# Performance work log

Hardware: AMD Instinct MI355X
Metric: run time of the kernel (lower is better)

Reference implementation:

```python
import jax, jax.numpy as jnp
import numpy as np

B, N, R = 16, 512, 10
DE, DR, DOUT = 256, 64, 256

def setup_inputs() -> dict:
    key = jax.random.key(0)
    k1, k2, k3, k4 = jax.random.split(key, 4)
    node_features = jax.random.normal(k1, (B, N, DE), dtype=jnp.float32)
    relation_features = jax.random.normal(k2, (B, R, DR), dtype=jnp.float32)
    adj = jax.random.uniform(k3, (B, R, N, N), dtype=jnp.float32)
    in_dim = (DE + DR) * R
    bound = float(np.sqrt(6.0 / (in_dim + DOUT)))  # xavier_uniform
    W = jax.random.uniform(k4, (DOUT, in_dim), dtype=jnp.float32, minval=-bound, maxval=bound)
    bias = jnp.zeros((DOUT,), dtype=jnp.float32)
    return {"node_features": node_features, "relation_features": relation_features,
            "adj": adj, "W": W, "bias": bias}

def reference(node_features, relation_features, adj, W, bias):
    # adj: [B,R,N,N]; node_features: [B,N,De]; relation_features: [B,R,Dr]
    # Per relation r: bmm(adj[:,r], cat([node, rel_r broadcast], -1))
    # Node part: adj @ node_features for every relation at once.
    node_part = jnp.einsum('brnm,bmd->brnd', adj, node_features)      # [B,R,N,De]
    # Relation part: adj @ (rel_r repeated over rows) == rowsum(adj) * rel_r
    rel_part = adj.sum(axis=-1)[..., None] * relation_features[:, :, None, :]  # [B,R,N,Dr]
    supports = jnp.concatenate([node_part, rel_part], axis=-1)        # [B,R,N,De+Dr]
    supports = supports.transpose(0, 2, 1, 3).reshape(node_features.shape[0],
                                                      node_features.shape[1], -1)  # [B,N,R*(De+Dr)]
    return supports @ W.T + bias
```

## Files before the change

kernel.cpp:

```cpp
#include <hip/hip_runtime.h>
#include <stdint.h>

#define B_     16
#define N_     512
#define R_     10
#define DE_    256
#define DR_    64
#define DOUT_  256
#define INDIM_ 3200
#define BLK_   320
#define RN_    5120
#define SPLITS_ 4
#define CPS_    20

typedef __bf16          v8bf  __attribute__((ext_vector_type(8)));
typedef unsigned short  v8us  __attribute__((ext_vector_type(8)));
typedef unsigned short  v4us  __attribute__((ext_vector_type(4)));
typedef float           f32x4 __attribute__((ext_vector_type(4)));

static __device__ __forceinline__ unsigned short f2b(float f) {
  union { float f; unsigned u; } c; c.f = f;
  unsigned r = c.u + 0x7FFFu + ((c.u >> 16) & 1u);
  return (unsigned short)(r >> 16);
}

static __device__ __forceinline__ v8bf us2bf(v8us u) {
  union { v8us u; v8bf b; } c; c.u = u; return c.b;
}

static __device__ __forceinline__ void gl_lds16(const void* g, void* l) {
  __builtin_amdgcn_global_load_lds(
      (const __attribute__((address_space(1))) void*)g,
      (__attribute__((address_space(3))) void*)l, 16, 0, 0);
}

__global__ void prep_all(const float* __restrict__ nf, const float* __restrict__ W,
                         const float* __restrict__ rel,
                         unsigned short* __restrict__ nodeB,
                         unsigned short* __restrict__ WnB,
                         float* __restrict__ Uf) {
  const int bb = blockIdx.x;
  const int tid = threadIdx.x;
  if (bb < 256) {
    const size_t base = (size_t)bb * 8192;
#pragma unroll
    for (int p = 0; p < 4; ++p) {
      size_t off = base + (size_t)p * 2048 + (size_t)tid * 8;
      float4 x = *(const float4*)(nf + off);
      float4 y = *(const float4*)(nf + off + 4);
      v8us u;
      u[0] = f2b(x.x); u[1] = f2b(x.y); u[2] = f2b(x.z); u[3] = f2b(x.w);
      u[4] = f2b(y.x); u[5] = f2b(y.y); u[6] = f2b(y.z); u[7] = f2b(y.w);
      *(v8us*)(nodeB + off) = u;
    }
  } else if (bb < 896) {
    int idx = (bb - 256) * 1024 + tid * 4;
    int r = idx >> 16;
    int o = (idx >> 8) & 255;
    int d = idx & 255;
    float4 x = *(const float4*)(W + (size_t)o * INDIM_ + r * BLK_ + d);
    v4us u;
    u[0] = f2b(x.x); u[1] = f2b(x.y); u[2] = f2b(x.z); u[3] = f2b(x.w);
    *(v4us*)(WnB + idx) = u;
  } else {
    int idx = (bb - 896) * 256 + tid;
    int o  = idx & 255;
    int br = idx >> 8;
    int r  = br % R_;
    const float* rp = rel + (size_t)br * DR_;
    const float* wp = W + (size_t)o * INDIM_ + r * BLK_ + DE_;
    float v = 0.f;
#pragma unroll 8
    for (int d = 0; d < DR_; ++d) v += rp[d] * wp[d];
    Uf[idx] = v;
  }
}

__global__ void stageA_gemm(const unsigned short* __restrict__ nodeB,
                            const unsigned short* __restrict__ WnB,
                            const float* __restrict__ Uf,
                            unsigned short* __restrict__ Gp) {
  __shared__ unsigned short S[128 * 128];
  unsigned short* Al = S;
  unsigned short* Bl = S + 128 * 64;
  const int br = blockIdx.x;
  const int b  = br / R_, r = br % R_;
  const int o0 = blockIdx.y * 128;
  const int m0 = blockIdx.z * 128;
  const int tid  = threadIdx.x;
  const int lane = tid & 63;
  const int wave = tid >> 6;
  const int wm = wave >> 1, wn = wave & 1;
  const int quad = lane >> 4, l16 = lane & 15;

  const unsigned short* Wb = WnB + (size_t)r * (DOUT_ * DE_);
  const unsigned short* Nb = nodeB + (size_t)b * (N_ * DE_);

  f32x4 acc[4][4];
#pragma unroll
  for (int i = 0; i < 4; ++i)
#pragma unroll
    for (int j = 0; j < 4; ++j) acc[i][j] = f32x4{0.f, 0.f, 0.f, 0.f};

  for (int dk = 0; dk < DE_; dk += 64) {
#pragma unroll
    for (int it = 0; it < 4; ++it) {
      int rowblk = it * 32 + wave * 8;
      int rl = rowblk + (lane >> 3);
      int kc = (lane & 7) ^ (rl & 7);
      gl_lds16(Wb + (size_t)(o0 + rl) * DE_ + dk + kc * 8, Al + rowblk * 64);
      gl_lds16(Nb + (size_t)(m0 + rl) * DE_ + dk + kc * 8, Bl + rowblk * 64);
    }
    __syncthreads();
#pragma unroll
    for (int ks = 0; ks < 2; ++ks) {
      const int kb = ks * 4;
      v8bf av[4], bv[4];
#pragma unroll
      for (int mi = 0; mi < 4; ++mi) {
        int m = wm * 64 + mi * 16 + l16;
        av[mi] = us2bf(*(const v8us*)(Al + m * 64 + (((kb + quad) ^ (m & 7)) * 8)));
      }
#pragma unroll
      for (int ni = 0; ni < 4; ++ni) {
        int c = wn * 64 + ni * 16 + l16;
        bv[ni] = us2bf(*(const v8us*)(Bl + c * 64 + (((kb + quad) ^ (c & 7)) * 8)));
      }
#pragma unroll
      for (int mi = 0; mi < 4; ++mi)
#pragma unroll
        for (int ni = 0; ni < 4; ++ni)
          acc[mi][ni] = __builtin_amdgcn_mfma_f32_16x16x32_bf16(av[mi], bv[ni], acc[mi][ni], 0, 0, 0);
    }
    __syncthreads();
  }

#pragma unroll
  for (int mi = 0; mi < 4; ++mi)
#pragma unroll
    for (int t = 0; t < 4; ++t) {
      int o_loc = wm * 64 + mi * 16 + quad * 4 + t;
      float u = Uf[(size_t)br * DOUT_ + o0 + o_loc];
#pragma unroll
      for (int ni = 0; ni < 4; ++ni) {
        int m_loc = wn * 64 + ni * 16 + l16;
        S[o_loc * 128 + m_loc] = f2b(acc[mi][ni][t] + u);
      }
    }
  __syncthreads();
#pragma unroll
  for (int p = 0; p < 8; ++p) {
    int idx16 = p * 2048 + tid * 8;
    int orow = idx16 >> 7;
    int moff = idx16 & 127;
    unsigned short* dst = Gp + ((size_t)(b * DOUT_ + o0 + orow)) * RN_ + r * N_ + m0 + moff;
    *(v8us*)dst = *(const v8us*)(S + idx16);
  }
}

__global__ __launch_bounds__(512, 2)
void stageB_gemm(const float* __restrict__ adj,
                 const unsigned short* __restrict__ Gp,
                 float* __restrict__ part) {
  __shared__ unsigned short SB[2 * 24576];
  const int b  = blockIdx.x;
  const int n0 = blockIdx.y * 128;
  const int sp = blockIdx.z;
  const int tid  = threadIdx.x;
  const int lane = tid & 63;
  const int wave = tid >> 6;
  const int wm = wave >> 2;
  const int wn = wave & 3;
  const int quad = lane >> 4, l16 = lane & 15;

  const float* Ab = adj + (size_t)b * (R_ * N_ * N_);
  const unsigned short* Gb = Gp + (size_t)b * (DOUT_ * RN_);

  f32x4 acc[4][4];
#pragma unroll
  for (int i = 0; i < 4; ++i)
#pragma unroll
    for (int j = 0; j < 4; ++j) acc[i][j] = f32x4{0.f, 0.f, 0.f, 0.f};

  const int ar0 = tid >> 3;
  const int ac8 = tid & 7;
  const int acs = ac8 ^ (ar0 & 7);
  const int brl = wave * 8 + (lane >> 3);
  const int bkc = lane & 7;

  int c = sp * CPS_;

  {
    const int r = c >> 3, m0 = (c & 7) << 6, k0 = c << 6;
    unsigned short* Aln = SB;
    unsigned short* Bln = SB + 128 * 64;
#pragma unroll
    for (int s = 0; s < 4; ++s) {
      int rl = s * 64 + brl;
      int kc = bkc ^ (rl & 7);
      gl_lds16(Gb + (size_t)rl * RN_ + k0 + kc * 8, Bln + (s * 64 + wave * 8) * 64);
    }
    const float* Ap = Ab + ((size_t)r * N_ + n0) * N_ + m0;
    float4 a0 = *(const float4*)(Ap + (size_t)ar0 * N_ + ac8 * 8);
    float4 a1 = *(const float4*)(Ap + (size_t)ar0 * N_ + ac8 * 8 + 4);
    float4 a2 = *(const float4*)(Ap + (size_t)(ar0 + 64) * N_ + ac8 * 8);
    float4 a3 = *(const float4*)(Ap + (size_t)(ar0 + 64) * N_ + ac8 * 8 + 4);
    v8us u0, u1;
    u0[0] = f2b(a0.x); u0[1] = f2b(a0.y); u0[2] = f2b(a0.z); u0[3] = f2b(a0.w);
    u0[4] = f2b(a1.x); u0[5] = f2b(a1.y); u0[6] = f2b(a1.z); u0[7] = f2b(a1.w);
    u1[0] = f2b(a2.x); u1[1] = f2b(a2.y); u1[2] = f2b(a2.z); u1[3] = f2b(a2.w);
    u1[4] = f2b(a3.x); u1[5] = f2b(a3.y); u1[6] = f2b(a3.z); u1[7] = f2b(a3.w);
    *(v8us*)(Aln + ar0 * 64 + acs * 8) = u0;
    *(v8us*)(Aln + (ar0 + 64) * 64 + acs * 8) = u1;
  }
  __syncthreads();

  for (int t = 0; t < CPS_; ++t) {
    unsigned short* Sc = SB + (t & 1) * 24576;
    unsigned short* Sn = SB + ((t & 1) ^ 1) * 24576;
    float4 a0, a1, a2, a3;
    const bool pf = (t + 1 < CPS_);
    if (pf) {
      const int c1 = c + 1;
      const int r = c1 >> 3, m0 = (c1 & 7) << 6, k0 = c1 << 6;
      unsigned short* Bln = Sn + 128 * 64;
#pragma unroll
      for (int s = 0; s < 4; ++s) {
        int rl = s * 64 + brl;
        int kc = bkc ^ (rl & 7);
        gl_lds16(Gb + (size_t)rl * RN_ + k0 + kc * 8, Bln + (s * 64 + wave * 8) * 64);
      }
      const float* Ap = Ab + ((size_t)r * N_ + n0) * N_ + m0;
      a0 = *(const float4*)(Ap + (size_t)ar0 * N_ + ac8 * 8);
      a1 = *(const float4*)(Ap + (size_t)ar0 * N_ + ac8 * 8 + 4);
      a2 = *(const float4*)(Ap + (size_t)(ar0 + 64) * N_ + ac8 * 8);
      a3 = *(const float4*)(Ap + (size_t)(ar0 + 64) * N_ + ac8 * 8 + 4);
    }
    const unsigned short* Alc = Sc;
    const unsigned short* Blc = Sc + 128 * 64;
#pragma unroll
    for (int ks = 0; ks < 2; ++ks) {
      const int kb = ks * 4;
      v8bf av[4], bv[4];
#pragma unroll
      for (int mi = 0; mi < 4; ++mi) {
        int m = wm * 64 + mi * 16 + l16;
        av[mi] = us2bf(*(const v8us*)(Alc + m * 64 + (((kb + quad) ^ (m & 7)) * 8)));
      }
#pragma unroll
      for (int ni = 0; ni < 4; ++ni) {
        int o = wn * 64 + ni * 16 + l16;
        bv[ni] = us2bf(*(const v8us*)(Blc + o * 64 + (((kb + quad) ^ (o & 7)) * 8)));
      }
#pragma unroll
      for (int mi = 0; mi < 4; ++mi)
#pragma unroll
        for (int ni = 0; ni < 4; ++ni)
          acc[mi][ni] = __builtin_amdgcn_mfma_f32_16x16x32_bf16(av[mi], bv[ni], acc[mi][ni], 0, 0, 0);
    }
    if (pf) {
      v8us u0, u1;
      u0[0] = f2b(a0.x); u0[1] = f2b(a0.y); u0[2] = f2b(a0.z); u0[3] = f2b(a0.w);
      u0[4] = f2b(a1.x); u0[5] = f2b(a1.y); u0[6] = f2b(a1.z); u0[7] = f2b(a1.w);
      u1[0] = f2b(a2.x); u1[1] = f2b(a2.y); u1[2] = f2b(a2.z); u1[3] = f2b(a2.w);
      u1[4] = f2b(a3.x); u1[5] = f2b(a3.y); u1[6] = f2b(a3.z); u1[7] = f2b(a3.w);
      *(v8us*)(Sn + ar0 * 64 + acs * 8) = u0;
      *(v8us*)(Sn + (ar0 + 64) * 64 + acs * 8) = u1;
    }
    __syncthreads();
    ++c;
  }

  float* pb = part + (((size_t)sp * B_ + b) * N_) * DOUT_;
#pragma unroll
  for (int mi = 0; mi < 4; ++mi)
#pragma unroll
    for (int t4 = 0; t4 < 4; ++t4) {
      int row = n0 + wm * 64 + mi * 16 + quad * 4 + t4;
#pragma unroll
      for (int ni = 0; ni < 4; ++ni) {
        int col = wn * 64 + ni * 16 + l16;
        pb[(size_t)row * DOUT_ + col] = acc[mi][ni][t4];
      }
    }
}

__global__ void reduce_out(const float* __restrict__ part, const float* __restrict__ bias,
                           float* __restrict__ out) {
  const size_t idx = (size_t)blockIdx.x * 256 + threadIdx.x;
  const size_t stride = (size_t)B_ * N_ * DOUT_ / 4;
  f32x4 a = *(const f32x4*)(bias + (idx & 63) * 4);
#pragma unroll
  for (int s = 0; s < SPLITS_; ++s) {
    f32x4 p = *(const f32x4*)((const float*)part + (stride * s + idx) * 4);
    a += p;
  }
  *(f32x4*)(out + idx * 4) = a;
}

extern "C" void kernel_launch(void* const* d_in, const int* in_sizes, int n_in,
                              void* d_out, int out_size, void* d_ws, size_t ws_size,
                              hipStream_t stream) {
  const float* node = (const float*)d_in[0];
  const float* rel  = (const float*)d_in[1];
  const float* adj  = (const float*)d_in[2];
  const float* W    = (const float*)d_in[3];
  const float* bias = (const float*)d_in[4];
  float* out = (float*)d_out;

  char* ws = (char*)d_ws;
  unsigned short* nodeB = (unsigned short*)(ws);
  unsigned short* WnB   = (unsigned short*)(ws + ((size_t)5 << 20));
  float*          Uf    = (float*)         (ws + ((size_t)7 << 20));
  unsigned short* Gp    = (unsigned short*)(ws + ((size_t)8 << 20));
  float*          part  = (float*)         (ws + ((size_t)48 << 20));

  prep_all<<<dim3(1056), 256, 0, stream>>>(node, W, rel, nodeB, WnB, Uf);
  stageA_gemm<<<dim3(B_ * R_, DOUT_ / 128, N_ / 128), 256, 0, stream>>>(nodeB, WnB, Uf, Gp);
  stageB_gemm<<<dim3(B_, N_ / 128, SPLITS_), 512, 0, stream>>>(adj, Gp, part);
  reduce_out<<<dim3((B_ * N_ * DOUT_ / 4) / 256), 256, 0, stream>>>(part, bias, out);
}
```

Baseline: 291.1 us.

## Double-buffer stage A K-loop and shrink stage B tiles to 64 rows

Stage A now double-buffers its LDS tiles across the four 64-wide K steps, prefetching the next chunk while MFMAs run on the current one. Stage B shrinks the row tile from 128 to 64 with 256-thread blocks, doubling the grid to 512 blocks so more CUs have work. Each wave in stage B now covers 64 output columns. The cost is that each block loads the full 256-column Gp tile for only 64 adjacency rows, so Gp is re-read twice as often.

```diff
diff --git a/kernel.cpp b/kernel.cpp
--- a/kernel.cpp
+++ b/kernel.cpp
@@ -80,9 +80,7 @@
                             const unsigned short* __restrict__ WnB,
                             const float* __restrict__ Uf,
                             unsigned short* __restrict__ Gp) {
-  __shared__ unsigned short S[128 * 128];
-  unsigned short* Al = S;
-  unsigned short* Bl = S + 128 * 64;
+  __shared__ unsigned short S[2 * 16384];
   const int br = blockIdx.x;
   const int b  = br / R_, r = br % R_;
   const int o0 = blockIdx.y * 128;
@@ -102,16 +100,41 @@
 #pragma unroll
     for (int j = 0; j < 4; ++j) acc[i][j] = f32x4{0.f, 0.f, 0.f, 0.f};
 
-  for (int dk = 0; dk < DE_; dk += 64) {
+  const int srl = lane >> 3;
+  const int skc = lane & 7;
+
+  {
+    unsigned short* Al = S;
+    unsigned short* Bl = S + 8192;
 #pragma unroll
     for (int it = 0; it < 4; ++it) {
       int rowblk = it * 32 + wave * 8;
-      int rl = rowblk + (lane >> 3);
-      int kc = (lane & 7) ^ (rl & 7);
-      gl_lds16(Wb + (size_t)(o0 + rl) * DE_ + dk + kc * 8, Al + rowblk * 64);
-      gl_lds16(Nb + (size_t)(m0 + rl) * DE_ + dk + kc * 8, Bl + rowblk * 64);
-    }
-    __syncthreads();
+      int rl = rowblk + srl;
+      int kc = skc ^ (rl & 7);
+      gl_lds16(Wb + (size_t)(o0 + rl) * DE_ + kc * 8, Al + rowblk * 64);
+      gl_lds16(Nb + (size_t)(m0 + rl) * DE_ + kc * 8, Bl + rowblk * 64);
+    }
+  }
+  __syncthreads();
+
+  for (int t = 0; t < 4; ++t) {
+    unsigned short* Sc = S + (t & 1) * 16384;
+    unsigned short* Sn = S + ((t & 1) ^ 1) * 16384;
+    if (t < 3) {
+      const int dk = (t + 1) * 64;
+      unsigned short* Aln = Sn;
+      unsigned short* Bln = Sn + 8192;
+#pragma unroll
+      for (int it = 0; it < 4; ++it) {
+        int rowblk = it * 32 + wave * 8;
+        int rl = rowblk + srl;
+        int kc = skc ^ (rl & 7);
+        gl_lds16(Wb + (size_t)(o0 + rl) * DE_ + dk + kc * 8, Aln + rowblk * 64);
+        gl_lds16(Nb + (size_t)(m0 + rl) * DE_ + dk + kc * 8, Bln + rowblk * 64);
+      }
+    }
+    const unsigned short* Al = Sc;
+    const unsigned short* Bl = Sc + 8192;
 #pragma unroll
     for (int ks = 0; ks < 2; ++ks) {
       const int kb = ks * 4;
@@ -158,19 +181,17 @@
   }
 }
 
-__global__ __launch_bounds__(512, 2)
+__global__ __launch_bounds__(256, 2)
 void stageB_gemm(const float* __restrict__ adj,
                  const unsigned short* __restrict__ Gp,
                  float* __restrict__ part) {
-  __shared__ unsigned short SB[2 * 24576];
+  __shared__ unsigned short SB[2 * 20480];
   const int b  = blockIdx.x;
-  const int n0 = blockIdx.y * 128;
+  const int n0 = blockIdx.y * 64;
   const int sp = blockIdx.z;
   const int tid  = threadIdx.x;
   const int lane = tid & 63;
   const int wave = tid >> 6;
-  const int wm = wave >> 2;
-  const int wn = wave & 3;
   const int quad = lane >> 4, l16 = lane & 15;
 
   const float* Ab = adj + (size_t)b * (R_ * N_ * N_);
@@ -182,74 +203,75 @@
 #pragma unroll
     for (int j = 0; j < 4; ++j) acc[i][j] = f32x4{0.f, 0.f, 0.f, 0.f};
 
-  const int ar0 = tid >> 3;
-  const int ac8 = tid & 7;
-  const int acs = ac8 ^ (ar0 & 7);
+  const int ar   = tid >> 2;
+  const int ac16 = tid & 3;
+  const int sl0  = (ac16 * 2) ^ (ar & 7);
+  const int sl1  = (ac16 * 2 + 1) ^ (ar & 7);
   const int brl = wave * 8 + (lane >> 3);
   const int bkc = lane & 7;
 
   int c = sp * CPS_;
 
   {
-    const int r = c >> 3, m0 = (c & 7) << 6, k0 = c << 6;
+    const int r = c >> 3, mc = (c & 7) << 6, k0 = c << 6;
     unsigned short* Aln = SB;
-    unsigned short* Bln = SB + 128 * 64;
-#pragma unroll
-    for (int s = 0; s < 4; ++s) {
-      int rl = s * 64 + brl;
+    unsigned short* Bln = SB + 4096;
+#pragma unroll
+    for (int s = 0; s < 8; ++s) {
+      int rl = s * 32 + brl;
       int kc = bkc ^ (rl & 7);
-      gl_lds16(Gb + (size_t)rl * RN_ + k0 + kc * 8, Bln + (s * 64 + wave * 8) * 64);
-    }
-    const float* Ap = Ab + ((size_t)r * N_ + n0) * N_ + m0;
-    float4 a0 = *(const float4*)(Ap + (size_t)ar0 * N_ + ac8 * 8);
-    float4 a1 = *(const float4*)(Ap + (size_t)ar0 * N_ + ac8 * 8 + 4);
-    float4 a2 = *(const float4*)(Ap + (size_t)(ar0 + 64) * N_ + ac8 * 8);
-    float4 a3 = *(const float4*)(Ap + (size_t)(ar0 + 64) * N_ + ac8 * 8 + 4);
+      gl_lds16(Gb + (size_t)rl * RN_ + k0 + kc * 8, Bln + (s * 32 + wave * 8) * 64);
+    }
+    const float* Ap = Ab + ((size_t)r * N_ + n0) * N_ + mc + (size_t)ar * N_ + ac16 * 16;
+    float4 a0 = *(const float4*)(Ap);
+    float4 a1 = *(const float4*)(Ap + 4);
+    float4 a2 = *(const float4*)(Ap + 8);
+    float4 a3 = *(const float4*)(Ap + 12);
     v8us u0, u1;
     u0[0] = f2b(a0.x); u0[1] = f2b(a0.y); u0[2] = f2b(a0.z); u0[3] = f2b(a0.w);
     u0[4] = f2b(a1.x); u0[5] = f2b(a1.y); u0[6] = f2b(a1.z); u0[7] = f2b(a1.w);
     u1[0] = f2b(a2.x); u1[1] = f2b(a2.y); u1[2] = f2b(a2.z); u1[3] = f2b(a2.w);
     u1[4] = f2b(a3.x); u1[5] = f2b(a3.y); u1[6] = f2b(a3.z); u1[7] = f2b(a3.w);
-    *(v8us*)(Aln + ar0 * 64 + acs * 8) = u0;
-    *(v8us*)(Aln + (ar0 + 64) * 64 + acs * 8) = u1;
+    *(v8us*)(Aln + ar * 64 + sl0 * 8) = u0;
+    *(v8us*)(Aln + ar * 64 + sl1 * 8) = u1;
   }
   __syncthreads();
 
   for (int t = 0; t < CPS_; ++t) {
-    unsigned short* Sc = SB + (t & 1) * 24576;
-    unsigned short* Sn = SB + ((t & 1) ^ 1) * 24576;
+    unsigned short* Sc = SB + (t & 1) * 20480;
+    unsigned short* Sn = SB + ((t & 1) ^ 1) * 20480;
     float4 a0, a1, a2, a3;
     const bool pf = (t + 1 < CPS_);
     if (pf) {
       const int c1 = c + 1;
-      const int r = c1 >> 3, m0 = (c1 & 7) << 6, k0 = c1 << 6;
-      unsigned short* Bln = Sn + 128 * 64;
-#pragma unroll
-      for (int s = 0; s < 4; ++s) {
-        int rl = s * 64 + brl;
+      const int r = c1 >> 3, mc = (c1 & 7) << 6, k0 = c1 << 6;
+      unsigned short* Bln = Sn + 4096;
+#pragma unroll
+      for (int s = 0; s < 8; ++s) {
+        int rl = s * 32 + brl;
         int kc = bkc ^ (rl & 7);
-        gl_lds16(Gb + (size_t)rl * RN_ + k0 + kc * 8, Bln + (s * 64 + wave * 8) * 64);
-      }
-      const float* Ap = Ab + ((size_t)r * N_ + n0) * N_ + m0;
-      a0 = *(const float4*)(Ap + (size_t)ar0 * N_ + ac8 * 8);
-      a1 = *(const float4*)(Ap + (size_t)ar0 * N_ + ac8 * 8 + 4);
-      a2 = *(const float4*)(Ap + (size_t)(ar0 + 64) * N_ + ac8 * 8);
-      a3 = *(const float4*)(Ap + (size_t)(ar0 + 64) * N_ + ac8 * 8 + 4);
+        gl_lds16(Gb + (size_t)rl * RN_ + k0 + kc * 8, Bln + (s * 32 + wave * 8) * 64);
+      }
+      const float* Ap = Ab + ((size_t)r * N_ + n0) * N_ + mc + (size_t)ar * N_ + ac16 * 16;
+      a0 = *(const float4*)(Ap);
+      a1 = *(const float4*)(Ap + 4);
+      a2 = *(const float4*)(Ap + 8);
+      a3 = *(const float4*)(Ap + 12);
     }
     const unsigned short* Alc = Sc;
-    const unsigned short* Blc = Sc + 128 * 64;
+    const unsigned short* Blc = Sc + 4096;
 #pragma unroll
     for (int ks = 0; ks < 2; ++ks) {
       const int kb = ks * 4;
       v8bf av[4], bv[4];
 #pragma unroll
       for (int mi = 0; mi < 4; ++mi) {
-        int m = wm * 64 + mi * 16 + l16;
+        int m = mi * 16 + l16;
         av[mi] = us2bf(*(const v8us*)(Alc + m * 64 + (((kb + quad) ^ (m & 7)) * 8)));
       }
 #pragma unroll
       for (int ni = 0; ni < 4; ++ni) {
-        int o = wn * 64 + ni * 16 + l16;
+        int o = wave * 64 + ni * 16 + l16;
         bv[ni] = us2bf(*(const v8us*)(Blc + o * 64 + (((kb + quad) ^ (o & 7)) * 8)));
       }
 #pragma unroll
@@ -264,8 +286,8 @@
       u0[4] = f2b(a1.x); u0[5] = f2b(a1.y); u0[6] = f2b(a1.z); u0[7] = f2b(a1.w);
       u1[0] = f2b(a2.x); u1[1] = f2b(a2.y); u1[2] = f2b(a2.z); u1[3] = f2b(a2.w);
       u1[4] = f2b(a3.x); u1[5] = f2b(a3.y); u1[6] = f2b(a3.z); u1[7] = f2b(a3.w);
-      *(v8us*)(Sn + ar0 * 64 + acs * 8) = u0;
-      *(v8us*)(Sn + (ar0 + 64) * 64 + acs * 8) = u1;
+      *(v8us*)(Sn + ar * 64 + sl0 * 8) = u0;
+      *(v8us*)(Sn + ar * 64 + sl1 * 8) = u1;
     }
     __syncthreads();
     ++c;
@@ -276,10 +298,10 @@
   for (int mi = 0; mi < 4; ++mi)
 #pragma unroll
     for (int t4 = 0; t4 < 4; ++t4) {
-      int row = n0 + wm * 64 + mi * 16 + quad * 4 + t4;
+      int row = n0 + mi * 16 + quad * 4 + t4;
 #pragma unroll
       for (int ni = 0; ni < 4; ++ni) {
-        int col = wn * 64 + ni * 16 + l16;
+        int col = wave * 64 + ni * 16 + l16;
         pb[(size_t)row * DOUT_ + col] = acc[mi][ni][t4];
       }
     }
@@ -317,6 +339,6 @@
 
   prep_all<<<dim3(1056), 256, 0, stream>>>(node, W, rel, nodeB, WnB, Uf);
   stageA_gemm<<<dim3(B_ * R_, DOUT_ / 128, N_ / 128), 256, 0, stream>>>(nodeB, WnB, Uf, Gp);
-  stageB_gemm<<<dim3(B_, N_ / 128, SPLITS_), 512, 0, stream>>>(adj, Gp, part);
+  stageB_gemm<<<dim3(B_, N_ / 64, SPLITS_), 256, 0, stream>>>(adj, Gp, part);
   reduce_out<<<dim3((B_ * N_ * DOUT_ / 4) / 256), 256, 0, stream>>>(part, bias, out);
 }
```

Result: no change. 295.7 us (+1.6%).
